# Optimization experiments

Measured on AMD Instinct MI355X. Metric: run time of the kernel, lower is better.

Reference implementation:

```python
import jax, jax.numpy as jnp
import numpy as np

D, H, FF, E, K, B, S = 1024, 16, 4096, 8, 2, 2, 2048
EPS = 1e-5


def _layernorm(x, g, b):
    mu = x.mean(-1, keepdims=True)
    var = x.var(-1, keepdims=True)
    return (x - mu) * jax.lax.rsqrt(var + EPS) * g + b


def setup_inputs() -> dict:
    key = jax.random.key(0)
    ks = jax.random.split(key, 16)
    s = 0.02
    return {
        "x": jax.random.normal(ks[0], (B, S, D), dtype=jnp.float32),
        "in_proj_w": jax.random.normal(ks[1], (3 * D, D), dtype=jnp.float32) * s,
        "in_proj_b": jnp.zeros((3 * D,), jnp.float32),
        "out_proj_w": jax.random.normal(ks[2], (D, D), dtype=jnp.float32) * s,
        "out_proj_b": jnp.zeros((D,), jnp.float32),
        "ln1_g": jnp.ones((D,), jnp.float32),
        "ln1_b": jnp.zeros((D,), jnp.float32),
        "ln2_g": jnp.ones((D,), jnp.float32),
        "ln2_b": jnp.zeros((D,), jnp.float32),
        "gate_w": jax.random.normal(ks[3], (E, D), dtype=jnp.float32) * s,
        "gate_b": jnp.zeros((E,), jnp.float32),
        "w1": jax.random.normal(ks[4], (E, FF, D), dtype=jnp.float32) * s,
        "b1": jnp.zeros((E, FF), jnp.float32),
        "w2": jax.random.normal(ks[5], (E, D, FF), dtype=jnp.float32) * s,
        "b2": jnp.zeros((E, D), jnp.float32),
    }


def reference(x, in_proj_w, in_proj_b, out_proj_w, out_proj_b,
              ln1_g, ln1_b, ln2_g, ln2_b,
              gate_w, gate_b, w1, b1, w2, b2):
    b, s, d = x.shape
    hd = d // H
    # --- self-attention (pre-LN), dropout = identity (eval) ---
    normed = _layernorm(x, ln1_g, ln1_b)
    qkv = normed @ in_proj_w.T + in_proj_b            # [b,s,3d]
    q, k, v = jnp.split(qkv, 3, axis=-1)
    q = q.reshape(b, s, H, hd).transpose(0, 2, 1, 3)  # [b,h,s,hd]
    k = k.reshape(b, s, H, hd).transpose(0, 2, 1, 3)
    v = v.reshape(b, s, H, hd).transpose(0, 2, 1, 3)
    scores = jnp.einsum('bhqe,bhke->bhqk', q, k) / np.sqrt(hd)
    attn = jax.nn.softmax(scores, axis=-1)
    o = jnp.einsum('bhqk,bhke->bhqe', attn, v)
    o = o.transpose(0, 2, 1, 3).reshape(b, s, d)
    attn_out = o @ out_proj_w.T + out_proj_b
    x = x + attn_out
    present_kv = (normed, normed)
    # --- MoE FFN ---
    n2 = _layernorm(x, ln2_g, ln2_b)
    xf = n2.reshape(-1, d)                             # [T,d]
    T = xf.shape[0]
    logits = xf @ gate_w.T + gate_b                    # [T,E]
    probs = jax.nn.softmax(logits, axis=-1)
    top_v, top_i = jax.lax.top_k(probs, K)             # [T,K]
    top_v = top_v / top_v.sum(-1, keepdims=True)
    # combine weights per (token, expert); topk indices are unique per token
    cw = jnp.zeros((T, E), probs.dtype).at[jnp.arange(T)[:, None], top_i].add(top_v)
    # dense all-experts FFN (mathematically identical to masked gather/scatter)
    h = jnp.einsum('td,efd->etf', xf, w1) + b1[:, None, :]   # [E,T,FF]
    h = jax.nn.gelu(h, approximate=False)
    eo = jnp.einsum('etf,edf->etd', h, w2) + b2[:, None, :]  # [E,T,d]
    moe_out = jnp.einsum('te,etd->td', cw, eo)               # [T,d]
    out = x + moe_out.reshape(b, s, d)
    # --- load balance loss (Switch) ---
    top1 = jnp.argmax(probs, axis=-1)
    f = jnp.mean(jax.nn.one_hot(top1, E, dtype=probs.dtype), axis=0)
    P = probs.mean(axis=0)
    load_loss = 0.01 * E * jnp.sum(f * P)
    return out, load_loss, probs.reshape(b, s, E), present_kv[0]
```

## Files before the change

kernel.cpp:

```cpp
#include <hip/hip_runtime.h>
#include <math.h>

#define D_ 1024
#define H_ 16
#define HD_ 64
#define FF_ 4096
#define E_ 8
#define B_ 2
#define S_ 2048
#define T_ 4096
#define MAXROWS 9216
#define MAXTILES 72

typedef unsigned short u16;
typedef __attribute__((ext_vector_type(4))) float f32x4;
typedef __attribute__((ext_vector_type(8))) __bf16 bf16x8;
typedef __attribute__((ext_vector_type(8))) _Float16 f16x8;
typedef __attribute__((ext_vector_type(4))) unsigned short u16x4;

__device__ __forceinline__ u16 f2bf(float f){
  union { float f; unsigned u; } v; v.f = f;
  unsigned r = v.u + 0x7fffu + ((v.u >> 16) & 1u);
  return (u16)(r >> 16);
}
__device__ __forceinline__ float bf2f(u16 h){
  union { unsigned u; float f; } v; v.u = ((unsigned)h) << 16;
  return v.f;
}
__device__ __forceinline__ void glds16(const void* g, void* l){
  __builtin_amdgcn_global_load_lds((const __attribute__((address_space(1))) void*)g,
                                   (__attribute__((address_space(3))) void*)l, 16, 0, 0);
}
__device__ __forceinline__ bf16x8 ld8(const u16* p){
  return *reinterpret_cast<const bf16x8*>(p);
}
__device__ __forceinline__ f16x8 ldH8(const _Float16* p){
  return *reinterpret_cast<const f16x8*>(p);
}
__device__ __forceinline__ f32x4 mfma16(bf16x8 a, bf16x8 b, f32x4 c){
  return __builtin_amdgcn_mfma_f32_16x16x32_bf16(a, b, c, 0, 0, 0);
}
__device__ __forceinline__ f32x4 mfmaH(f16x8 a, f16x8 b, f32x4 c){
  return __builtin_amdgcn_mfma_f32_16x16x32_f16(a, b, c, 0, 0, 0);
}
__device__ __forceinline__ unsigned pk16(float a, float b){
  auto pk = __builtin_amdgcn_cvt_pkrtz(a, b);
  return __builtin_bit_cast(unsigned, pk);
}

__global__ void __launch_bounds__(256) split_hl_kernel(const float* __restrict__ in, u16* __restrict__ hi,
                                                       u16* __restrict__ lo, int n4){
  int i = blockIdx.x*blockDim.x + threadIdx.x;
  if (i >= n4) return;
  float4 v = reinterpret_cast<const float4*>(in)[i];
  float vv[4] = {v.x, v.y, v.z, v.w};
  u16x4 h, l;
  #pragma unroll
  for (int j=0;j<4;j++){
    u16 hh = f2bf(vv[j]);
    h[j] = hh;
    l[j] = f2bf(vv[j] - bf2f(hh));
  }
  reinterpret_cast<u16x4*>(hi)[i] = h;
  reinterpret_cast<u16x4*>(lo)[i] = l;
}

__global__ void __launch_bounds__(256) cvt_bf_kernel(const float* __restrict__ in, u16* __restrict__ out, int n4){
  int i = blockIdx.x*blockDim.x + threadIdx.x;
  if (i >= n4) return;
  float4 v = reinterpret_cast<const float4*>(in)[i];
  u16x4 o;
  o[0]=f2bf(v.x); o[1]=f2bf(v.y); o[2]=f2bf(v.z); o[3]=f2bf(v.w);
  reinterpret_cast<u16x4*>(out)[i] = o;
}

__global__ void __launch_bounds__(256) cvt_f16_kernel(const float* __restrict__ in, _Float16* __restrict__ out, int n4){
  int i = blockIdx.x*blockDim.x + threadIdx.x;
  if (i >= n4) return;
  float4 v = reinterpret_cast<const float4*>(in)[i];
  union { unsigned w[2]; u16x4 u; } o;
  o.w[0] = pk16(v.x, v.y);
  o.w[1] = pk16(v.z, v.w);
  reinterpret_cast<u16x4*>(out)[i] = o.u;
}

template<int OUTMODE, int GATE>
__global__ void __launch_bounds__(256) ln_kernel(const float* __restrict__ x, const float* __restrict__ g,
    const float* __restrict__ bta, float* __restrict__ outf, u16* __restrict__ nout,
    const float* __restrict__ gw, const float* __restrict__ gb,
    float* __restrict__ probs_out, int* __restrict__ top_i, float* __restrict__ cw_w)
{
  const int t = blockIdx.x, tid = threadIdx.x;
  __shared__ float rs[4], rq[4];
  __shared__ float sp[4][E_];
  const float4 v = reinterpret_cast<const float4*>(x + (size_t)t*D_)[tid];
  float s  = v.x+v.y+v.z+v.w;
  float s2 = v.x*v.x+v.y*v.y+v.z*v.z+v.w*v.w;
  #pragma unroll
  for (int o=32;o;o>>=1){ s += __shfl_xor(s,o); s2 += __shfl_xor(s2,o); }
  const int wid=tid>>6, lane=tid&63;
  if (lane==0){ rs[wid]=s; rq[wid]=s2; }
  __syncthreads();
  s  = rs[0]+rs[1]+rs[2]+rs[3];
  s2 = rq[0]+rq[1]+rq[2]+rq[3];
  const float mu  = s*(1.0f/D_);
  const float var = s2*(1.0f/D_) - mu*mu;
  const float inv = rsqrtf(var + 1e-5f);
  const float4 gv = reinterpret_cast<const float4*>(g)[tid];
  const float4 bv = reinterpret_cast<const float4*>(bta)[tid];
  float oo[4];
  oo[0] = (v.x-mu)*inv*gv.x + bv.x;
  oo[1] = (v.y-mu)*inv*gv.y + bv.y;
  oo[2] = (v.z-mu)*inv*gv.z + bv.z;
  oo[3] = (v.w-mu)*inv*gv.w + bv.w;
  const size_t base = (size_t)t*D_ + tid*4;
  if (outf){ outf[base]=oo[0]; outf[base+1]=oo[1]; outf[base+2]=oo[2]; outf[base+3]=oo[3]; }
  if (OUTMODE==1){
    union { unsigned w[2]; u16x4 u; } hv;
    hv.w[0] = pk16(oo[0], oo[1]);
    hv.w[1] = pk16(oo[2], oo[3]);
    reinterpret_cast<u16x4*>(nout)[base>>2] = hv.u;
  } else {
    u16x4 hv;
    hv[0]=f2bf(oo[0]); hv[1]=f2bf(oo[1]); hv[2]=f2bf(oo[2]); hv[3]=f2bf(oo[3]);
    reinterpret_cast<u16x4*>(nout)[base>>2] = hv;
  }
  if (GATE){
    float part[E_];
    #pragma unroll
    for (int e=0;e<E_;e++){
      const float4 wv = reinterpret_cast<const float4*>(gw + (size_t)e*D_)[tid];
      part[e] = oo[0]*wv.x + oo[1]*wv.y + oo[2]*wv.z + oo[3]*wv.w;
    }
    #pragma unroll
    for (int e=0;e<E_;e++){
      #pragma unroll
      for (int o=32;o;o>>=1) part[e] += __shfl_xor(part[e], o);
    }
    if (lane==0){
      #pragma unroll
      for (int e=0;e<E_;e++) sp[wid][e] = part[e];
    }
    __syncthreads();
    if (tid==0){
      float lg[E_], mx=-3e38f;
      #pragma unroll
      for (int e=0;e<E_;e++){
        lg[e] = sp[0][e]+sp[1][e]+sp[2][e]+sp[3][e] + gb[e];
        mx = fmaxf(mx, lg[e]);
      }
      float ex[E_], sm=0.f;
      #pragma unroll
      for (int e=0;e<E_;e++){ ex[e]=__expf(lg[e]-mx); sm+=ex[e]; }
      float p[E_];
      #pragma unroll
      for (int e=0;e<E_;e++){ p[e]=ex[e]/sm; probs_out[(size_t)t*E_+e]=p[e]; }
      int i0=0; float l0=lg[0];
      #pragma unroll
      for (int e=1;e<E_;e++) if (lg[e]>l0){ l0=lg[e]; i0=e; }
      int i1=-1; float l1=-3e38f;
      #pragma unroll
      for (int e=0;e<E_;e++) if (e!=i0 && lg[e]>l1){ l1=lg[e]; i1=e; }
      top_i[2*t]=i0; top_i[2*t+1]=i1;
      const float v0=p[i0], v1=p[i1];
      const float swt=v0+v1;
      cw_w[2*t]=v0/swt; cw_w[2*t+1]=v1/swt;
    }
  }
}

__global__ void __launch_bounds__(256) qkv_kernel(
    const _Float16* __restrict__ A, const _Float16* __restrict__ Bw,
    const float* __restrict__ bias,
    _Float16* __restrict__ qf, _Float16* __restrict__ kf, _Float16* __restrict__ vtf)
{
  __shared__ __align__(16) _Float16 Ash[2][128*32], Bsh[2][128*32];
  const int bid = blockIdx.x, nwg = gridDim.x;
  const int fid = (bid & 7)*(nwg>>3) + (bid>>3);
  const int nt = fid % 24, mt = fid / 24;
  const int tid=threadIdx.x, wid=tid>>6, lane=tid&63;
  const int wr=wid>>1, wc=wid&1;
  const int r16=lane&15, g4=lane>>4;
  const _Float16* Ag = A  + (size_t)mt*128*D_;
  const _Float16* Bg = Bw + (size_t)nt*128*D_;
  const int srow = wid*16 + (lane>>2);
  const int scol = (((lane&3) ^ ((lane>>3)&3)))*8;
  const int sl   = (g4 ^ ((r16>>1)&3))*8;
  f32x4 acc[4][4] = {};
#define QSTAGE(bi, k0) do { \
    _Pragma("unroll") \
    for (int p=0;p<2;p++){ \
      const int r  = p*64 + srow; \
      const int lo = (p*64 + wid*16)*32; \
      glds16(Ag + (size_t)r*D_ + (k0) + scol, &Ash[bi][lo]); \
      glds16(Bg + (size_t)r*D_ + (k0) + scol, &Bsh[bi][lo]); \
    } \
  } while(0)
  QSTAGE(0, 0);
  int cur = 0;
  for (int t=0; t<D_/32; ++t){
    if (t+1 < D_/32){
      QSTAGE(cur^1, (t+1)*32);
      asm volatile("s_waitcnt vmcnt(4)" ::: "memory");
    } else {
      asm volatile("s_waitcnt vmcnt(0)" ::: "memory");
    }
    __syncthreads();
    f16x8 af[4], bfr[4];
    #pragma unroll
    for (int m=0;m<4;m++) af[m]=ldH8(&Ash[cur][(wr*64+m*16+r16)*32 + sl]);
    #pragma unroll
    for (int n=0;n<4;n++) bfr[n]=ldH8(&Bsh[cur][(wc*64+n*16+r16)*32 + sl]);
    #pragma unroll
    for (int m=0;m<4;m++){
      #pragma unroll
      for (int n=0;n<4;n++) acc[m][n] = mfmaH(af[m], bfr[n], acc[m][n]);
    }
    __syncthreads();
    cur ^= 1;
  }
#undef QSTAGE
  #pragma unroll
  for (int m=0;m<4;m++){
    #pragma unroll
    for (int n=0;n<4;n++){
      #pragma unroll
      for (int r=0;r<4;r++){
        const int grow = mt*128 + wr*64 + m*16 + g4*4 + r;
        const int gcol = nt*128 + wc*64 + n*16 + r16;
        const float val = acc[m][n][r] + bias[gcol];
        const int which = gcol>>10, rem = gcol&1023;
        const int hh = rem>>6, ee = rem&63;
        const int bb = grow>>11, ss = grow&2047;
        if (which==0){
          qf[((size_t)(bb*H_+hh)*S_ + ss)*HD_ + ee] = (_Float16)(val * 0.18033688f);
        } else if (which==1){
          kf[((size_t)(bb*H_+hh)*S_ + ss)*HD_ + ee] = (_Float16)val;
        } else {
          const int p32 = 2*(ss & 12) + (ss & 3) + 4*((ss >> 4) & 1);
          const size_t idx = (((size_t)(bb*H_+hh)*(S_/32) + (ss>>5))*HD_ + ee)*32 + p32;
          vtf[idx] = (_Float16)val;
        }
      }
    }
  }
}

__global__ void __launch_bounds__(256) gemm3_kernel(
    const u16* __restrict__ Ah, const u16* __restrict__ Al, int lda,
    const u16* __restrict__ Bh, const u16* __restrict__ Bl, int Kdim,
    const float* __restrict__ bias,
    const float* __restrict__ resid, float* __restrict__ x1out)
{
  __shared__ __align__(16) u16 Ash[2][128*32], Asl[2][128*32], Bsh[2][128*32], Bsl[2][128*32];
  const int bid = blockIdx.x, nwg = gridDim.x;
  const int fid = (bid & 7)*(nwg>>3) + (bid>>3);
  const int nt = fid & 7, mt = fid >> 3;
  const int tid=threadIdx.x, wid=tid>>6, lane=tid&63;
  const int wr=wid>>1, wc=wid&1;
  const int r16=lane&15, g4=lane>>4;
  const u16* Agh = Ah + (size_t)mt*128*lda;
  const u16* Agl = Al + (size_t)mt*128*lda;
  const u16* Bgh = Bh + (size_t)nt*128*Kdim;
  const u16* Bgl = Bl + (size_t)nt*128*Kdim;
  const int srow = wid*16 + (lane>>2);
  const int scol = (((lane&3) ^ ((lane>>3)&3)))*8;
  const int sl   = (g4 ^ ((r16>>1)&3))*8;
  f32x4 acc[4][4] = {};
#define G3STAGE(bi, k0) do { \
    _Pragma("unroll") \
    for (int p=0;p<2;p++){ \
      const int r  = p*64 + srow; \
      const int lo = (p*64 + wid*16)*32; \
      glds16(Agh + (size_t)r*lda  + (k0) + scol, &Ash[bi][lo]); \
      glds16(Agl + (size_t)r*lda  + (k0) + scol, &Asl[bi][lo]); \
      glds16(Bgh + (size_t)r*Kdim + (k0) + scol, &Bsh[bi][lo]); \
      glds16(Bgl + (size_t)r*Kdim + (k0) + scol, &Bsl[bi][lo]); \
    } \
  } while(0)
  G3STAGE(0, 0);
  int cur = 0;
  const int NK = Kdim/32;
  for (int t=0; t<NK; ++t){
    if (t+1 < NK){
      G3STAGE(cur^1, (t+1)*32);
      asm volatile("s_waitcnt vmcnt(8)" ::: "memory");
    } else {
      asm volatile("s_waitcnt vmcnt(0)" ::: "memory");
    }
    __syncthreads();
    bf16x8 afh[4], afl[4], bfh[4], bfl[4];
    #pragma unroll
    for (int m=0;m<4;m++){
      const int row = wr*64 + m*16 + r16;
      afh[m] = ld8(&Ash[cur][row*32 + sl]);
      afl[m] = ld8(&Asl[cur][row*32 + sl]);
    }
    #pragma unroll
    for (int n=0;n<4;n++){
      const int row = wc*64 + n*16 + r16;
      bfh[n] = ld8(&Bsh[cur][row*32 + sl]);
      bfl[n] = ld8(&Bsl[cur][row*32 + sl]);
    }
    #pragma unroll
    for (int m=0;m<4;m++){
      #pragma unroll
      for (int n=0;n<4;n++){
        acc[m][n] = mfma16(afl[m], bfh[n], acc[m][n]);
        acc[m][n] = mfma16(afh[m], bfl[n], acc[m][n]);
        acc[m][n] = mfma16(afh[m], bfh[n], acc[m][n]);
      }
    }
    __syncthreads();
    cur ^= 1;
  }
#undef G3STAGE
  #pragma unroll
  for (int m=0;m<4;m++){
    #pragma unroll
    for (int n=0;n<4;n++){
      #pragma unroll
      for (int r=0;r<4;r++){
        const int grow = mt*128 + wr*64 + m*16 + g4*4 + r;
        const int gcol = nt*128 + wc*64 + n*16 + r16;
        const float val = acc[m][n][r] + bias[gcol];
        const size_t idx = (size_t)grow*D_ + gcol;
        x1out[idx] = val + resid[idx];
      }
    }
  }
}

__global__ void __launch_bounds__(256) attn9_kernel(
    const _Float16* __restrict__ Qf, const _Float16* __restrict__ Kf,
    const _Float16* __restrict__ Vtf,
    u16* __restrict__ Oh, u16* __restrict__ Ol)
{
  __shared__ __align__(16) _Float16 Kb[2][4096];
  __shared__ __align__(16) _Float16 Vb[2][4096];
  const int bid = blockIdx.x;
  const int wg = (bid & 7) * 128 + (bid >> 3);
  const int bh = wg >> 5, qc = wg & 31;
  const int tid=threadIdx.x, wid=tid>>6, lane=tid&63;
  const int r16=lane&15, g4=lane>>4;
  const int q0 = qc*64 + wid*16;
  const _Float16* Qp = Qf  + (size_t)bh*S_*HD_ + (size_t)(q0+r16)*HD_ + g4*8;
  const _Float16* Kbase = Kf  + (size_t)bh*S_*HD_;
  const _Float16* Vbase = Vtf + (size_t)bh*HD_*S_;
  const f16x8 qf0 = ldH8(Qp);
  const f16x8 qf1 = ldH8(Qp+32);
  f32x4 of[4] = {};
  float m_run = -3e38f, lr = 0.f;

  const int kOff = (wid*8 + (lane>>3))*HD_ + (((lane&7) ^ ((lane>>3)&7)))*8;
  const int vOff = wid*512 + lane*8;
  const int sk0 = (g4 ^ (r16&7))*8;
  const int sk1 = ((g4+4) ^ (r16&7))*8;

#define STAGE(bi, tt) do { \
    glds16(Kbase + (size_t)(tt)*64*HD_ + kOff,          (void*)&Kb[bi][wid*512]); \
    glds16(Kbase + (size_t)(tt)*64*HD_ + 32*HD_ + kOff, (void*)&Kb[bi][2048 + wid*512]); \
    glds16(Vbase + (size_t)(tt)*4096 + vOff,            (void*)&Vb[bi][wid*512]); \
    glds16(Vbase + (size_t)(tt)*4096 + 2048 + vOff,     (void*)&Vb[bi][2048 + wid*512]); \
  } while(0)

#define ATT_HALF(Kh_, Vh_) do { \
    const f16x8 k0v = ldH8((Kh_) + r16*64 + sk0); \
    const f16x8 k1v = ldH8((Kh_) + r16*64 + sk1); \
    const f16x8 k2v = ldH8((Kh_) + (16+r16)*64 + sk0); \
    const f16x8 k3v = ldH8((Kh_) + (16+r16)*64 + sk1); \
    f32x4 sA={}, sB={}; \
    __builtin_amdgcn_s_setprio(1); \
    sA = mfmaH(k0v, qf0, sA); sA = mfmaH(k1v, qf1, sA); \
    sB = mfmaH(k2v, qf0, sB); sB = mfmaH(k3v, qf1, sB); \
    __builtin_amdgcn_s_setprio(0); \
    const float t0=sA[0], t1=sA[1], t2=sA[2], t3=sA[3]; \
    const float t4=sB[0], t5=sB[1], t6=sB[2], t7=sB[3]; \
    const float lmx = fmaxf(fmaxf(fmaxf(t0,t1),fmaxf(t2,t3)), \
                            fmaxf(fmaxf(t4,t5),fmaxf(t6,t7))); \
    if (!__all(lmx <= m_run + 4.0f)) { \
      float mx = fmaxf(lmx, __shfl_xor(lmx,16)); \
      mx = fmaxf(mx, __shfl_xor(mx,32)); \
      const float mn = fmaxf(m_run, mx); \
      const float alp = __builtin_amdgcn_exp2f(m_run - mn); \
      m_run = mn; \
      lr *= alp; \
      const float ao0=__shfl(alp,4*g4), ao1=__shfl(alp,4*g4+1); \
      const float ao2=__shfl(alp,4*g4+2), ao3=__shfl(alp,4*g4+3); \
      _Pragma("unroll") \
      for (int c=0;c<4;c++){ of[c][0]*=ao0; of[c][1]*=ao1; of[c][2]*=ao2; of[c][3]*=ao3; } \
    } \
    const float msh = m_run - 9.0f; \
    const float p0=__builtin_amdgcn_exp2f(t0-msh), p1=__builtin_amdgcn_exp2f(t1-msh); \
    const float p2=__builtin_amdgcn_exp2f(t2-msh), p3=__builtin_amdgcn_exp2f(t3-msh); \
    const float p4=__builtin_amdgcn_exp2f(t4-msh), p5=__builtin_amdgcn_exp2f(t5-msh); \
    const float p6=__builtin_amdgcn_exp2f(t6-msh), p7=__builtin_amdgcn_exp2f(t7-msh); \
    lr += ((p0+p1)+(p2+p3)) + ((p4+p5)+(p6+p7)); \
    union { unsigned w[4]; f16x8 v; } pu; \
    pu.w[0]=pk16(p0,p1); pu.w[1]=pk16(p2,p3); \
    pu.w[2]=pk16(p4,p5); pu.w[3]=pk16(p6,p7); \
    const f16x8 v0v = ldH8((Vh_) + (r16)*32 + g4*8); \
    const f16x8 v1v = ldH8((Vh_) + (16+r16)*32 + g4*8); \
    const f16x8 v2v = ldH8((Vh_) + (32+r16)*32 + g4*8); \
    const f16x8 v3v = ldH8((Vh_) + (48+r16)*32 + g4*8); \
    __builtin_amdgcn_s_setprio(1); \
    of[0] = mfmaH(pu.v, v0v, of[0]); of[1] = mfmaH(pu.v, v1v, of[1]); \
    of[2] = mfmaH(pu.v, v2v, of[2]); of[3] = mfmaH(pu.v, v3v, of[3]); \
    __builtin_amdgcn_s_setprio(0); \
  } while(0)

  STAGE(0, 0);
  int cur = 0;

  for (int t=0; t<32; ++t){
    if (t < 31){
      STAGE(cur^1, t+1);
      asm volatile("s_waitcnt vmcnt(4)" ::: "memory");
    } else {
      asm volatile("s_waitcnt vmcnt(0)" ::: "memory");
    }
    __syncthreads();
    ATT_HALF(&Kb[cur][0],    &Vb[cur][0]);
    ATT_HALF(&Kb[cur][2048], &Vb[cur][2048]);
    __syncthreads();
    cur ^= 1;
  }
#undef ATT_HALF
#undef STAGE

  lr += __shfl_xor(lr,16);
  lr += __shfl_xor(lr,32);
  float li[4];
  #pragma unroll
  for (int r=0;r<4;r++) li[r] = 1.0f / __shfl(lr, 4*g4+r);
  const int bb = bh>>4, hh = bh&15;
  #pragma unroll
  for (int c=0;c<4;c++){
    #pragma unroll
    for (int r=0;r<4;r++){
      const float val = of[c][r] * li[r];
      const int qq = q0 + 4*g4 + r;
      const size_t idx = ((size_t)(bb*S_+qq))*D_ + hh*HD_ + c*16 + r16;
      const u16 hi = f2bf(val);
      Oh[idx]=hi; Ol[idx]=f2bf(val-bf2f(hi));
    }
  }
}

__global__ void __launch_bounds__(512) scan_kernel(const int* __restrict__ top_i,
    int* __restrict__ goff, int* __restrict__ tile_expert,
    int* __restrict__ assign_token, int* __restrict__ pos_of)
{
  __shared__ int cnt[E_];
  __shared__ int off[E_+1];
  const int tid=threadIdx.x;
  if (tid<E_) cnt[tid]=0;
  __syncthreads();
  for (int t=tid;t<T_;t+=512){
    atomicAdd(&cnt[top_i[2*t]],1);
    atomicAdd(&cnt[top_i[2*t+1]],1);
  }
  __syncthreads();
  if (tid==0){
    off[0]=0;
    for (int e=0;e<E_;e++) off[e+1]=off[e]+((cnt[e]+127)&~127);
    for (int i=0;i<=E_;i++) goff[i]=off[i];
  }
  __syncthreads();
  if (tid<MAXTILES){
    const int r=tid*128; int e=-1;
    for (int j=0;j<E_;j++) if (r>=off[j] && r<off[j+1]) e=j;
    tile_expert[tid]=e;
  }
  const int lane=tid&63;
  const int e=tid>>6;
  int base=off[e];
  for (int c=0;c<T_/64;c++){
    const int t=c*64+lane;
    const int a0=top_i[2*t], a1=top_i[2*t+1];
    const bool f=(a0==e)||(a1==e);
    const unsigned long long m=__ballot(f);
    if (f){
      const int pos = base + (int)__popcll(m & ((1ull<<lane)-1ull));
      assign_token[pos]=t;
      pos_of[2*t + (a0==e?0:1)] = pos;
    }
    base += (int)__popcll(m);
  }
  for (int r=base+lane; r<off[e+1]; r+=64) assign_token[r]=-1;
  __syncthreads();
  for (int r=off[E_]+tid; r<MAXROWS; r+=512) assign_token[r]=-1;
}

__global__ void __launch_bounds__(256) gather_kernel(const int* __restrict__ assign_token,
    const u16* __restrict__ n2b, u16* __restrict__ xg)
{
  const int r = blockIdx.x;
  const int t = assign_token[r];
  u16x4 val = {};
  if (t>=0) val = reinterpret_cast<const u16x4*>(n2b + (size_t)t*D_)[threadIdx.x];
  reinterpret_cast<u16x4*>(xg + (size_t)r*D_)[threadIdx.x] = val;
}

template<int MODE>
__global__ void __launch_bounds__(256, 4) gemm_grp_kernel(
    const u16* __restrict__ A, int lda,
    const u16* __restrict__ Bbase, int Kdim, int Nsz, int NT,
    const float* __restrict__ bias,
    const int* __restrict__ tile_expert,
    u16* __restrict__ outp)
{
  const int bid = blockIdx.x, nwg = gridDim.x;
  const int fid = (bid & 7)*(nwg>>3) + (bid>>3);
  const int nt = fid % NT, mt = fid / NT;
  const int e = tile_expert[mt];
  if (e<0) return;
  __shared__ __align__(16) u16 Ash[2][128*32], Bsh[2][128*32];
  const int tid=threadIdx.x, wid=tid>>6, lane=tid&63;
  const int wr=wid>>1, wc=wid&1;
  const int r16=lane&15, g4=lane>>4;
  const u16* Ag = A + (size_t)mt*128*lda;
  const u16* Bg = Bbase + (size_t)e*Nsz*Kdim + (size_t)nt*128*Kdim;
  const float* bp = bias + (size_t)e*Nsz;
  const int srow = wid*16 + (lane>>2);
  const int scol = (((lane&3) ^ ((lane>>3)&3)))*8;
  const int sl   = (g4 ^ ((r16>>1)&3))*8;
  f32x4 acc[4][4] = {};
#define GSTAGE(bi, k0) do { \
    _Pragma("unroll") \
    for (int p=0;p<2;p++){ \
      const int r  = p*64+srow; \
      const int lo = (p*64+wid*16)*32; \
      glds16(Ag + (size_t)r*lda  + (k0) + scol, &Ash[bi][lo]); \
      glds16(Bg + (size_t)r*Kdim + (k0) + scol, &Bsh[bi][lo]); \
    } \
  } while(0)
  GSTAGE(0, 0);
  int cur = 0;
  const int NK = Kdim/32;
  for (int t=0; t<NK; ++t){
    if (t+1 < NK){
      GSTAGE(cur^1, (t+1)*32);
      asm volatile("s_waitcnt vmcnt(4)" ::: "memory");
    } else {
      asm volatile("s_waitcnt vmcnt(0)" ::: "memory");
    }
    __syncthreads();
    bf16x8 af[4], bfr[4];
    #pragma unroll
    for (int m=0;m<4;m++) af[m]=ld8(&Ash[cur][(wr*64+m*16+r16)*32 + sl]);
    #pragma unroll
    for (int n=0;n<4;n++) bfr[n]=ld8(&Bsh[cur][(wc*64+n*16+r16)*32 + sl]);
    #pragma unroll
    for (int m=0;m<4;m++){
      #pragma unroll
      for (int n=0;n<4;n++) acc[m][n] = mfma16(af[m], bfr[n], acc[m][n]);
    }
    __syncthreads();
    cur ^= 1;
  }
#undef GSTAGE
  #pragma unroll
  for (int m=0;m<4;m++){
    #pragma unroll
    for (int n=0;n<4;n++){
      #pragma unroll
      for (int r=0;r<4;r++){
        const int grow = mt*128 + wr*64 + m*16 + g4*4 + r;
        const int gcol = nt*128 + wc*64 + n*16 + r16;
        float val = acc[m][n][r] + bp[gcol];
        if (MODE==2){
          const float z = val*(1.0f + 0.044715f*val*val)*2.3021622f;
          val = val / (1.0f + __builtin_amdgcn_exp2f(-z));
        }
        outp[(size_t)grow*Nsz + gcol] = f2bf(val);
      }
    }
  }
}

__global__ void __launch_bounds__(256) combine_kernel(const float* __restrict__ x1,
    const u16* __restrict__ eo, const int* __restrict__ pos_of, const float* __restrict__ cw_w,
    float* __restrict__ out0)
{
  const int t=blockIdx.x, tid=threadIdx.x;
  const int r0=pos_of[2*t], r1=pos_of[2*t+1];
  const float w0=cw_w[2*t], w1=cw_w[2*t+1];
  const u16x4 e0 = reinterpret_cast<const u16x4*>(eo + (size_t)r0*D_)[tid];
  const u16x4 e1 = reinterpret_cast<const u16x4*>(eo + (size_t)r1*D_)[tid];
  const float4 xv = reinterpret_cast<const float4*>(x1 + (size_t)t*D_)[tid];
  float4 o;
  o.x = xv.x + w0*bf2f(e0[0]) + w1*bf2f(e1[0]);
  o.y = xv.y + w0*bf2f(e0[1]) + w1*bf2f(e1[1]);
  o.z = xv.z + w0*bf2f(e0[2]) + w1*bf2f(e1[2]);
  o.w = xv.w + w0*bf2f(e0[3]) + w1*bf2f(e1[3]);
  reinterpret_cast<float4*>(out0 + (size_t)t*D_)[tid] = o;
}

__global__ void __launch_bounds__(256) loss_kernel(const float* __restrict__ probs,
    const int* __restrict__ top_i, float* __restrict__ loss_out)
{
  const int tid=threadIdx.x;
  float f[E_]={0,0,0,0,0,0,0,0}, P[E_]={0,0,0,0,0,0,0,0};
  for (int t=tid;t<T_;t+=256){
    const float* pr = probs + (size_t)t*E_;
    const int a0 = top_i[2*t];
    #pragma unroll
    for (int e=0;e<E_;e++){
      P[e] += pr[e];
      f[e] += (a0==e) ? 1.0f : 0.0f;
    }
  }
  #pragma unroll
  for (int e=0;e<E_;e++){
    #pragma unroll
    for (int o=32;o;o>>=1){ f[e]+=__shfl_xor(f[e],o); P[e]+=__shfl_xor(P[e],o); }
  }
  __shared__ float sf[4][E_], sP[4][E_];
  const int wid=tid>>6, lane=tid&63;
  if (lane==0){
    #pragma unroll
    for (int e=0;e<E_;e++){ sf[wid][e]=f[e]; sP[wid][e]=P[e]; }
  }
  __syncthreads();
  if (tid==0){
    float loss=0.f;
    #pragma unroll
    for (int e=0;e<E_;e++){
      const float fe=sf[0][e]+sf[1][e]+sf[2][e]+sf[3][e];
      const float Pe=sP[0][e]+sP[1][e]+sP[2][e]+sP[3][e];
      loss += (fe/(float)T_)*(Pe/(float)T_);
    }
    loss_out[0] = 0.01f*(float)E_*loss;
  }
}

static inline size_t alup(size_t x){ return (x+255)&~(size_t)255; }

extern "C" void kernel_launch(void* const* d_in, const int* in_sizes, int n_in,
                              void* d_out, int out_size, void* d_ws, size_t ws_size,
                              hipStream_t stream) {
  (void)in_sizes; (void)n_in; (void)out_size; (void)ws_size;
  const float* x    = (const float*)d_in[0];
  const float* ipw  = (const float*)d_in[1];
  const float* ipb  = (const float*)d_in[2];
  const float* opw  = (const float*)d_in[3];
  const float* opb  = (const float*)d_in[4];
  const float* ln1g = (const float*)d_in[5];
  const float* ln1b = (const float*)d_in[6];
  const float* ln2g = (const float*)d_in[7];
  const float* ln2b = (const float*)d_in[8];
  const float* gw   = (const float*)d_in[9];
  const float* gb   = (const float*)d_in[10];
  const float* w1   = (const float*)d_in[11];
  const float* b1   = (const float*)d_in[12];
  const float* w2   = (const float*)d_in[13];
  const float* b2   = (const float*)d_in[14];

  float* out0       = (float*)d_out;
  float* loss_out   = out0 + (size_t)T_*D_;
  float* probs_out  = loss_out + 1;
  float* normed_out = probs_out + (size_t)T_*E_;

  char* p = (char*)d_ws;
  auto take = [&](size_t bytes)->void*{ void* r = (void*)p; p += alup(bytes); return r; };

  _Float16* wipf = (_Float16*)take((size_t)3*D_*D_*2);
  u16* wop_h = (u16*)take((size_t)D_*D_*2);
  u16* wop_l = (u16*)take((size_t)D_*D_*2);
  u16* w1b   = (u16*)take((size_t)E_*FF_*D_*2);
  u16* w2b   = (u16*)take((size_t)E_*D_*FF_*2);
  _Float16* nf16 = (_Float16*)take((size_t)T_*D_*2);
  _Float16* qf  = (_Float16*)take((size_t)T_*D_*2);
  _Float16* kf  = (_Float16*)take((size_t)T_*D_*2);
  _Float16* vtf = (_Float16*)take((size_t)T_*D_*2);
  u16* oh    = (u16*)take((size_t)T_*D_*2);
  u16* ol    = (u16*)take((size_t)T_*D_*2);
  float* x1  = (float*)take((size_t)T_*D_*4);
  u16* n2b   = (u16*)take((size_t)T_*D_*2);
  u16* xg    = (u16*)take((size_t)MAXROWS*D_*2);
  u16* hbuf  = (u16*)take((size_t)MAXROWS*FF_*2);
  u16* eo    = (u16*)take((size_t)MAXROWS*D_*2);
  int* top_i = (int*)take((size_t)T_*2*4);
  float* cww = (float*)take((size_t)T_*2*4);
  int* posof = (int*)take((size_t)T_*2*4);
  int* goff  = (int*)take((size_t)(E_+1)*4);
  int* texp  = (int*)take((size_t)MAXTILES*4);
  int* atok  = (int*)take((size_t)MAXROWS*4);

  cvt_f16_kernel<<<(3*D_*D_/4+255)/256, 256, 0, stream>>>(ipw, wipf, 3*D_*D_/4);
  split_hl_kernel<<<(D_*D_/4+255)/256, 256, 0, stream>>>(opw, wop_h, wop_l, D_*D_/4);
  cvt_bf_kernel<<<(E_*FF_*D_/4+255)/256, 256, 0, stream>>>(w1, w1b, E_*FF_*D_/4);
  cvt_bf_kernel<<<(E_*D_*FF_/4+255)/256, 256, 0, stream>>>(w2, w2b, E_*D_*FF_/4);

  ln_kernel<1,0><<<T_, 256, 0, stream>>>(x, ln1g, ln1b, normed_out, (u16*)nf16,
                                         nullptr, nullptr, nullptr, nullptr, nullptr);

  qkv_kernel<<<dim3(24*(T_/128)), 256, 0, stream>>>(nf16, wipf, ipb, qf, kf, vtf);

  attn9_kernel<<<B_*H_*(S_/64), 256, 0, stream>>>(qf, kf, vtf, oh, ol);

  gemm3_kernel<<<dim3(8*(T_/128)), 256, 0, stream>>>(
      oh, ol, D_, wop_h, wop_l, D_, opb, x, x1);

  ln_kernel<2,1><<<T_, 256, 0, stream>>>(x1, ln2g, ln2b, nullptr, n2b,
                                         gw, gb, probs_out, top_i, cww);

  scan_kernel<<<1, 512, 0, stream>>>(top_i, goff, texp, atok, posof);

  gather_kernel<<<MAXROWS, 256, 0, stream>>>(atok, n2b, xg);

  gemm_grp_kernel<2><<<dim3((FF_/128)*MAXTILES), 256, 0, stream>>>(xg, D_, w1b, D_, FF_, FF_/128, b1, texp, hbuf);
  gemm_grp_kernel<3><<<dim3((D_/128)*MAXTILES), 256, 0, stream>>>(hbuf, FF_, w2b, FF_, D_, D_/128, b2, texp, eo);

  combine_kernel<<<T_, 256, 0, stream>>>(x1, eo, posof, cww, out0);
  loss_kernel<<<1, 256, 0, stream>>>(probs_out, top_i, loss_out);
}
```

Before: 539.6 us.

## Enlarge grouped MoE GEMM tiles to 256x256x64 with 512-thread blocks

The grouped expert GEMMs move from 128x128 tiles with K-step 32 and 256 threads to 256x256 tiles with K-step 64 and 512 threads (8 waves, each computing 128x64). Expert row padding changes to multiples of 256, with matching tile-expert mapping and buffer sizes. The LDS swizzle is reworked for 64-wide K rows, and s_setprio is set around the MFMA bursts. The aim is higher arithmetic intensity and fewer global loads per FLOP. The costs are more padding waste per expert, fewer blocks (possible tail effects on the grid), 128 KB of LDS per block, and a heavier register load that may lower occupancy.

```diff
diff --git a/kernel.cpp b/kernel.cpp
--- a/kernel.cpp
+++ b/kernel.cpp
@@ -9,8 +9,8 @@
 #define B_ 2
 #define S_ 2048
 #define T_ 4096
-#define MAXROWS 9216
-#define MAXTILES 72
+#define MAXROWS 10240
+#define MAXT256 40
 
 typedef unsigned short u16;
 typedef __attribute__((ext_vector_type(4))) float f32x4;
@@ -463,12 +463,12 @@
   __syncthreads();
   if (tid==0){
     off[0]=0;
-    for (int e=0;e<E_;e++) off[e+1]=off[e]+((cnt[e]+127)&~127);
+    for (int e=0;e<E_;e++) off[e+1]=off[e]+((cnt[e]+255)&~255);
     for (int i=0;i<=E_;i++) goff[i]=off[i];
   }
   __syncthreads();
-  if (tid<MAXTILES){
-    const int r=tid*128; int e=-1;
+  if (tid<MAXT256){
+    const int r=tid*256; int e=-1;
     for (int j=0;j<E_;j++) if (r>=off[j] && r<off[j+1]) e=j;
     tile_expert[tid]=e;
   }
@@ -503,7 +503,7 @@
 }
 
 template<int MODE>
-__global__ void __launch_bounds__(256, 4) gemm_grp_kernel(
+__global__ void __launch_bounds__(512, 2) gemm_grp_kernel(
     const u16* __restrict__ A, int lda,
     const u16* __restrict__ Bbase, int Kdim, int Nsz, int NT,
     const float* __restrict__ bias,
@@ -515,59 +515,66 @@
   const int nt = fid % NT, mt = fid / NT;
   const int e = tile_expert[mt];
   if (e<0) return;
-  __shared__ __align__(16) u16 Ash[2][128*32], Bsh[2][128*32];
+  __shared__ __align__(16) u16 Ash[2][256*64], Bsh[2][256*64];
   const int tid=threadIdx.x, wid=tid>>6, lane=tid&63;
-  const int wr=wid>>1, wc=wid&1;
+  const int wr=wid>>2, wc=wid&3;
   const int r16=lane&15, g4=lane>>4;
-  const u16* Ag = A + (size_t)mt*128*lda;
-  const u16* Bg = Bbase + (size_t)e*Nsz*Kdim + (size_t)nt*128*Kdim;
+  const u16* Ag = A + (size_t)mt*256*lda;
+  const u16* Bg = Bbase + (size_t)e*Nsz*Kdim + (size_t)nt*256*Kdim;
   const float* bp = bias + (size_t)e*Nsz;
-  const int srow = wid*16 + (lane>>2);
-  const int scol = (((lane&3) ^ ((lane>>3)&3)))*8;
-  const int sl   = (g4 ^ ((r16>>1)&3))*8;
-  f32x4 acc[4][4] = {};
+  const int srow8 = wid*8 + (lane>>3);
+  const int sc    = (((lane&7) ^ ((lane>>3)&7)))*8;
+  const int sk0 = (g4 ^ (r16&7))*8;
+  const int sk1 = ((4+g4) ^ (r16&7))*8;
+  f32x4 acc[8][4] = {};
 #define GSTAGE(bi, k0) do { \
     _Pragma("unroll") \
-    for (int p=0;p<2;p++){ \
-      const int r  = p*64+srow; \
-      const int lo = (p*64+wid*16)*32; \
-      glds16(Ag + (size_t)r*lda  + (k0) + scol, &Ash[bi][lo]); \
-      glds16(Bg + (size_t)r*Kdim + (k0) + scol, &Bsh[bi][lo]); \
+    for (int p=0;p<4;p++){ \
+      const int r  = p*64 + srow8; \
+      const int lo = (p*64 + wid*8)*64; \
+      glds16(Ag + (size_t)r*lda  + (k0) + sc, &Ash[bi][lo]); \
+      glds16(Bg + (size_t)r*Kdim + (k0) + sc, &Bsh[bi][lo]); \
     } \
   } while(0)
   GSTAGE(0, 0);
   int cur = 0;
-  const int NK = Kdim/32;
+  const int NK = Kdim/64;
   for (int t=0; t<NK; ++t){
     if (t+1 < NK){
-      GSTAGE(cur^1, (t+1)*32);
-      asm volatile("s_waitcnt vmcnt(4)" ::: "memory");
+      GSTAGE(cur^1, (t+1)*64);
+      asm volatile("s_waitcnt vmcnt(8)" ::: "memory");
     } else {
       asm volatile("s_waitcnt vmcnt(0)" ::: "memory");
     }
     __syncthreads();
-    bf16x8 af[4], bfr[4];
-    #pragma unroll
-    for (int m=0;m<4;m++) af[m]=ld8(&Ash[cur][(wr*64+m*16+r16)*32 + sl]);
-    #pragma unroll
-    for (int n=0;n<4;n++) bfr[n]=ld8(&Bsh[cur][(wc*64+n*16+r16)*32 + sl]);
-    #pragma unroll
-    for (int m=0;m<4;m++){
-      #pragma unroll
-      for (int n=0;n<4;n++) acc[m][n] = mfma16(af[m], bfr[n], acc[m][n]);
+    #pragma unroll
+    for (int kk=0;kk<2;kk++){
+      const int sl = kk ? sk1 : sk0;
+      bf16x8 af[8], bfr[4];
+      #pragma unroll
+      for (int m=0;m<8;m++) af[m]=ld8(&Ash[cur][(wr*128+m*16+r16)*64 + sl]);
+      #pragma unroll
+      for (int n=0;n<4;n++) bfr[n]=ld8(&Bsh[cur][(wc*64+n*16+r16)*64 + sl]);
+      __builtin_amdgcn_s_setprio(1);
+      #pragma unroll
+      for (int m=0;m<8;m++){
+        #pragma unroll
+        for (int n=0;n<4;n++) acc[m][n] = mfma16(af[m], bfr[n], acc[m][n]);
+      }
+      __builtin_amdgcn_s_setprio(0);
     }
     __syncthreads();
     cur ^= 1;
   }
 #undef GSTAGE
   #pragma unroll
-  for (int m=0;m<4;m++){
+  for (int m=0;m<8;m++){
     #pragma unroll
     for (int n=0;n<4;n++){
       #pragma unroll
       for (int r=0;r<4;r++){
-        const int grow = mt*128 + wr*64 + m*16 + g4*4 + r;
-        const int gcol = nt*128 + wc*64 + n*16 + r16;
+        const int grow = mt*256 + wr*128 + m*16 + g4*4 + r;
+        const int gcol = nt*256 + wc*64 + n*16 + r16;
         float val = acc[m][n][r] + bp[gcol];
         if (MODE==2){
           const float z = val*(1.0f + 0.044715f*val*val)*2.3021622f;
@@ -685,7 +692,7 @@
   float* cww = (float*)take((size_t)T_*2*4);
   int* posof = (int*)take((size_t)T_*2*4);
   int* goff  = (int*)take((size_t)(E_+1)*4);
-  int* texp  = (int*)take((size_t)MAXTILES*4);
+  int* texp  = (int*)take((size_t)MAXT256*4);
   int* atok  = (int*)take((size_t)MAXROWS*4);
 
   cvt_f16_kernel<<<(3*D_*D_/4+255)/256, 256, 0, stream>>>(ipw, wipf, 3*D_*D_/4);
@@ -710,8 +717,8 @@
 
   gather_kernel<<<MAXROWS, 256, 0, stream>>>(atok, n2b, xg);
 
-  gemm_grp_kernel<2><<<dim3((FF_/128)*MAXTILES), 256, 0, stream>>>(xg, D_, w1b, D_, FF_, FF_/128, b1, texp, hbuf);
-  gemm_grp_kernel<3><<<dim3((D_/128)*MAXTILES), 256, 0, stream>>>(hbuf, FF_, w2b, FF_, D_, D_/128, b2, texp, eo);
+  gemm_grp_kernel<2><<<dim3((FF_/256)*MAXT256), 512, 0, stream>>>(xg, D_, w1b, D_, FF_, FF_/256, b1, texp, hbuf);
+  gemm_grp_kernel<3><<<dim3((D_/256)*MAXT256), 512, 0, stream>>>(hbuf, FF_, w2b, FF_, D_, D_/256, b2, texp, eo);
 
   combine_kernel<<<T_, 256, 0, stream>>>(x1, eo, posof, cww, out0);
   loss_kernel<<<1, 256, 0, stream>>>(probs_out, top_i, loss_out);
```

Result: slower. 626.9 us (+16.2%).
